# Optimization experiments

Hardware: AMD Instinct MI355X
Metric: run time of the kernel (lower is better)

## Reference

```python
import jax, jax.numpy as jnp
import numpy as np

N, E, B, ROWS, IN, HID, JKO, FEAT, OH, OUT = 200000, 6400000, 64, 128, 128, 6, 4, 2560, 20, 2

def _leaky(x, s):
    return jnp.where(x >= 0, x, s * x)

def _ln(x, g, b, eps=1e-5):
    mu = jnp.mean(x, -1, keepdims=True)
    v = jnp.mean((x - mu) ** 2, -1, keepdims=True)
    return (x - mu) * jax.lax.rsqrt(v + eps) * g + b

def setup_inputs():
    key = jax.random.key(0)
    ks = jax.random.split(key, 32)
    def w(k, shape, fan_in):
        return jax.random.normal(k, shape, jnp.float32) * (1.0 / np.sqrt(fan_in))
    inp = {
        'x': jax.random.normal(ks[0], (N, IN), jnp.float32),
        'edge_index': jax.random.randint(ks[1], (2, E), 0, N, jnp.int32),
        'batch': jnp.sort(jax.random.randint(ks[2], (N,), 0, B, jnp.int32)),
        'features': jax.random.normal(ks[3], (B, ROWS, FEAT), jnp.float32),
        'one_hot': jax.random.uniform(ks[4], (B, OH), jnp.float32),
        # GATv2Conv params (heads=1)
        'W_l': w(ks[5], (IN, HID), IN), 'b_l': jnp.zeros((HID,)),
        'W_r': w(ks[6], (IN, HID), IN), 'b_r': jnp.zeros((HID,)),
        'att': w(ks[7], (HID,), HID), 'conv_b': jnp.zeros((HID,)),
        # BasicGNN final lin after JK (6 -> 4)
        'jk_W': w(ks[8], (HID, JKO), HID), 'jk_b': jnp.zeros((JKO,)),
        # MLP chain on features
        'l1_W': w(ks[9], (FEAT, 256), FEAT), 'l1_b': jnp.zeros((256,)),
        'ln1_g': jnp.ones((256,)), 'ln1_b': jnp.zeros((256,)),
        'l2_W': w(ks[10], (256, 64), 256), 'l2_b': jnp.zeros((64,)),
        'ln2_g': jnp.ones((64,)), 'ln2_b': jnp.zeros((64,)),
        'l3_W': w(ks[11], (64, 8), 64), 'l3_b': jnp.zeros((8,)),
        'ln3_g': jnp.ones((8,)), 'ln3_b': jnp.zeros((8,)),
        # flattening: rows*8 -> 32
        'fl_W': w(ks[12], (ROWS * 8, 32), ROWS * 8), 'fl_b': jnp.zeros((32,)),
        'ln4_g': jnp.ones((32,)), 'ln4_b': jnp.zeros((32,)),
        # output: 4 + 32 + 20 = 56 -> OUT
        'out_W': w(ks[13], (56, OUT), 56), 'out_b': jnp.zeros((OUT,)),
    }
    return inp

def _forward(x, features, one_hot, W_l, b_l, W_r, b_r, att, conv_b, jk_W, jk_b,
             l1_W, l1_b, ln1_g, ln1_b, l2_W, l2_b, ln2_g, ln2_b, l3_W, l3_b, ln3_g, ln3_b,
             fl_W, fl_b, ln4_g, ln4_b, out_W, out_b, edge_index, batch):
    n = x.shape[0]
    # GATv2Conv, heads=1: separate source/target transforms
    xl = x @ W_l + b_l  # [N,6] source/message features
    xr = x @ W_r + b_r  # [N,6] target features
    loops = jnp.arange(n, dtype=edge_index.dtype)
    src = jnp.concatenate([edge_index[0], loops])  # add self loops
    dst = jnp.concatenate([edge_index[1], loops])
    e = _leaky(xl[src] + xr[dst], 0.2)             # [E+N,6]
    score = e @ att                                 # [E+N]
    m = jax.lax.stop_gradient(jax.ops.segment_max(score, dst, num_segments=n))
    p = jnp.exp(score - m[dst])
    z = jax.ops.segment_sum(p, dst, num_segments=n)
    alpha = p / z[dst]                              # segment softmax over incoming edges
    agg = jax.ops.segment_sum(alpha[:, None] * xl[src], dst, num_segments=n) + conv_b
    x1 = _leaky(agg, 0.01)                          # BasicGNN act ('leakyrelu')
    # JK-LSTM with a single layer collapses to identity (softmax over 1 element)
    h = x1 @ jk_W + jk_b                            # [N,4]
    # global mean pool per graph
    nb = features.shape[0]
    sums = jax.ops.segment_sum(h, batch, num_segments=nb)
    cnt = jax.ops.segment_sum(jnp.ones((n,), h.dtype), batch, num_segments=nb)
    xgcn = sums / jnp.maximum(cnt, 1.0)[:, None]    # [B,4]
    # MLP on features (dropout = identity in eval)
    f = _leaky(_ln(features @ l1_W + l1_b, ln1_g, ln1_b), 0.01)
    f = _leaky(_ln(f @ l2_W + l2_b, ln2_g, ln2_b), 0.01)
    f = _leaky(_ln(f @ l3_W + l3_b, ln3_g, ln3_b), 0.01)  # [B,ROWS,8]
    flat = f.reshape(nb, -1)
    xf = _leaky(_ln(flat @ fl_W + fl_b, ln4_g, ln4_b), 0.01)  # [B,32]
    cat = jnp.concatenate([xgcn, xf, one_hot], axis=1)        # [B,56]
    return cat @ out_W + out_b

def reference(x, features, one_hot, W_l, b_l, W_r, b_r, att, conv_b, jk_W, jk_b,
              l1_W, l1_b, ln1_g, ln1_b, l2_W, l2_b, ln2_g, ln2_b, l3_W, l3_b, ln3_g, ln3_b,
              fl_W, fl_b, ln4_g, ln4_b, out_W, out_b, edge_index, batch):
    return _forward(x, features, one_hot, W_l, b_l, W_r, b_r, att, conv_b, jk_W, jk_b,
                    l1_W, l1_b, ln1_g, ln1_b, l2_W, l2_b, ln2_g, ln2_b, l3_W, l3_b, ln3_g, ln3_b,
                    fl_W, fl_b, ln4_g, ln4_b, out_W, out_b, edge_index, batch)
```

## Files before the change

kernel.cpp:

```cpp
#include <hip/hip_runtime.h>
#include <cstdint>
#include <cstddef>

#define N_NODES 200000
#define N_EDGES 6400000
#define NB      64
#define MROWS   8192
#define FEAT    2560

#define BSZ   256
#define NBK   782
#define EBLK  512
#define ETILE 12500
#define BCAP  8960

typedef __attribute__((ext_vector_type(8))) short bf16x8;
typedef __attribute__((ext_vector_type(4))) float f32x4;

__device__ __forceinline__ unsigned short bf16rne(float f) {
    unsigned u = __builtin_bit_cast(unsigned, f);
    u += 0x7fffu + ((u >> 16) & 1u);
    return (unsigned short)(u >> 16);
}

__device__ __forceinline__ void async_cp16(const void* g, void* l) {
    __builtin_amdgcn_global_load_lds(
        (const __attribute__((address_space(1))) unsigned int*)g,
        (__attribute__((address_space(3))) unsigned int*)l, 16, 0, 0);
}

__device__ __forceinline__ void edge_acc(
    uint4 g, const float* xrd, const float* attv, float& z, float* agg)
{
    float xls[6];
    xls[0] = __builtin_bit_cast(float, g.x << 16);
    xls[1] = __builtin_bit_cast(float, g.x & 0xffff0000u);
    xls[2] = __builtin_bit_cast(float, g.y << 16);
    xls[3] = __builtin_bit_cast(float, g.y & 0xffff0000u);
    xls[4] = __builtin_bit_cast(float, g.z << 16);
    xls[5] = __builtin_bit_cast(float, g.z & 0xffff0000u);
    float sc = 0.f;
#pragma unroll
    for (int j = 0; j < 6; j++) {
        float e = xls[j] + xrd[j];
        e = (e >= 0.f) ? e : 0.2f * e;
        sc += attv[j] * e;
    }
    const float p = __expf(sc);
    z += p;
#pragma unroll
    for (int j = 0; j < 6; j++) agg[j] += p * xls[j];
}


__global__ __launch_bounds__(256) void node_xform(
    const float* __restrict__ x,
    const float* __restrict__ Wl, const float* __restrict__ bl,
    const float* __restrict__ Wr, const float* __restrict__ br,
    unsigned short* __restrict__ xlb, float* __restrict__ xr)
{
    const int t = threadIdx.x;
    const int l = t & 15;
    const int node = blockIdx.x * 16 + (t >> 4);

    float wl[48], wr[48];
#pragma unroll
    for (int q = 0; q < 12; q++) {
        *(float4*)&wl[q * 4] = *(const float4*)(Wl + 48 * l + 4 * q);
        *(float4*)&wr[q * 4] = *(const float4*)(Wr + 48 * l + 4 * q);
    }
    float xv[8];
    *(float4*)&xv[0] = *(const float4*)(x + (size_t)node * 128 + l * 8);
    *(float4*)&xv[4] = *(const float4*)(x + (size_t)node * 128 + l * 8 + 4);

    float al[6] = {}, ar[6] = {};
#pragma unroll
    for (int i = 0; i < 8; i++) {
#pragma unroll
        for (int j = 0; j < 6; j++) {
            al[j] += xv[i] * wl[i * 6 + j];
            ar[j] += xv[i] * wr[i * 6 + j];
        }
    }
#pragma unroll
    for (int off = 8; off >= 1; off >>= 1) {
#pragma unroll
        for (int j = 0; j < 6; j++) {
            al[j] += __shfl_xor(al[j], off);
            ar[j] += __shfl_xor(ar[j], off);
        }
    }
    if (l == 0) {
        union { unsigned short h[8]; uint4 v; } u;
#pragma unroll
        for (int j = 0; j < 6; j++) u.h[j] = bf16rne(al[j] + bl[j]);
        u.h[6] = 0; u.h[7] = 0;
        *(uint4*)(xlb + (size_t)node * 8) = u.v;
        float4 r0; float2 r1;
        r0.x = ar[0] + br[0]; r0.y = ar[1] + br[1];
        r0.z = ar[2] + br[2]; r0.w = ar[3] + br[3];
        r1.x = ar[4] + br[4]; r1.y = ar[5] + br[5];
        *(float4*)(xr + (size_t)node * 8) = r0;
        *(float2*)(xr + (size_t)node * 8 + 4) = r1;
    }
}

__global__ __launch_bounds__(256) void edge_bucket(
    const int* __restrict__ ei, int* __restrict__ cursor, int* __restrict__ pairs)
{
    __shared__ int sorted[ETILE];
    __shared__ int hb[NBK + 1];
    __shared__ int cur[NBK];
    __shared__ int gbl[NBK];
    __shared__ int wsum[4];
    const int t = threadIdx.x;
    const int lane = t & 63, wid = t >> 6;
    const int base = blockIdx.x * ETILE;

    for (int b = t; b < NBK; b += 256) cur[b] = 0;
    __syncthreads();

    for (int i = t; i < ETILE; i += 256)
        atomicAdd(&cur[ei[N_EDGES + base + i] >> 8], 1);
    __syncthreads();

    int c[4]; int lsum = 0;
#pragma unroll
    for (int q = 0; q < 4; q++) {
        const int b = 4 * t + q;
        c[q] = (b < NBK) ? cur[b] : 0;
        lsum += c[q];
    }
    int v = lsum;
#pragma unroll
    for (int d = 1; d < 64; d <<= 1) {
        const int o = __shfl_up(v, d);
        if (lane >= d) v += o;
    }
    if (lane == 63) wsum[wid] = v;
    __syncthreads();
    int off = 0;
#pragma unroll
    for (int w = 0; w < 3; w++) if (w < wid) off += wsum[w];
    int run = off + v - lsum;

    int mygb[4];
#pragma unroll
    for (int q = 0; q < 4; q++) {
        const int b = 4 * t + q;
        mygb[q] = (b < NBK && c[q] > 0) ? atomicAdd(&cursor[b], c[q]) : 0;
    }

#pragma unroll
    for (int q = 0; q < 4; q++) {
        const int b = 4 * t + q;
        if (b <= NBK) hb[b] = run;
        if (b < NBK) cur[b] = run;
        run += c[q];
    }
    __syncthreads();

    for (int i = t; i < ETILE; i += 256) {
        const int d = ei[N_EDGES + base + i];
        const int s = ei[base + i];
        const int pos = atomicAdd(&cur[d >> 8], 1);
        sorted[pos] = (s << 8) | (d & 255);
    }
#pragma unroll
    for (int q = 0; q < 4; q++) {
        const int b = 4 * t + q;
        if (b < NBK) gbl[b] = mygb[q];
    }
    __syncthreads();

    const int grp = t >> 4, gl = t & 15;
    for (int b = grp; b < NBK; b += 16) {
        const int st = hb[b];
        const int cnt = hb[b + 1] - st;
        int* dst = pairs + b * BCAP + gbl[b];
        for (int i = gl; i < cnt; i += 16)
            dst[i] = sorted[st + i];
    }
}

__global__ __launch_bounds__(256) void bucket_reduce(
    const int* __restrict__ pairs, const int* __restrict__ cursor,
    const unsigned short* __restrict__ xlb, const float* __restrict__ xr,
    const float* __restrict__ att, const float* __restrict__ conv_b,
    const float* __restrict__ jkW, const float* __restrict__ jkb,
    const int* __restrict__ batch,
    float* __restrict__ gsum, float* __restrict__ gcnt)
{
    __shared__ int sorted[BCAP];
    __shared__ int hist[256];
    __shared__ int wtot[4];
    const int t = threadIdx.x;
    const int lane = t & 63, wid = t >> 6;
    const int d0 = blockIdx.x * BSZ + t;

    float xrd[6];
    if (d0 < N_NODES) {
        float4 a = *(const float4*)(xr + (size_t)d0 * 8);
        float2 b = *(const float2*)(xr + (size_t)d0 * 8 + 4);
        xrd[0] = a.x; xrd[1] = a.y; xrd[2] = a.z;
        xrd[3] = a.w; xrd[4] = b.x; xrd[5] = b.y;
    } else {
#pragma unroll
        for (int j = 0; j < 6; j++) xrd[j] = 0.f;
    }
    float attv[6];
#pragma unroll
    for (int j = 0; j < 6; j++) attv[j] = att[j];

    float z = 0.f, agg[6] = {};
    const uint4* xl4 = (const uint4*)xlb;
    const int e0 = blockIdx.x * BCAP;
    const int e1 = e0 + cursor[blockIdx.x];

    for (int c0 = e0; c0 < e1; c0 += BCAP) {
        const int rem = e1 - c0;
        const int cnt_chunk = (rem < BCAP) ? rem : BCAP;
        hist[t] = 0;
        __syncthreads();
        for (int i = t; i < cnt_chunk; i += 256)
            atomicAdd(&hist[pairs[c0 + i] & 255], 1);
        __syncthreads();
        const int h = hist[t];
        int v = h;
#pragma unroll
        for (int d = 1; d < 64; d <<= 1) {
            int o = __shfl_up(v, d);
            if (lane >= d) v += o;
        }
        if (lane == 63) wtot[wid] = v;
        __syncthreads();
        int off = 0;
#pragma unroll
        for (int wv = 0; wv < 3; wv++) if (wv < wid) off += wtot[wv];
        const int my_start = v - h + off;
        const int my_cnt = h;
        __syncthreads();
        hist[t] = my_start;
        __syncthreads();
        for (int i = t; i < cnt_chunk; i += 256) {
            const int pv = pairs[c0 + i];
            const int pos = atomicAdd(&hist[pv & 255], 1);
            sorted[pos] = ((unsigned)pv) >> 8;
        }
        __syncthreads();
        int i = 0;
        for (; i + 4 <= my_cnt; i += 4) {
            const int s0 = sorted[my_start + i];
            const int s1 = sorted[my_start + i + 1];
            const int s2 = sorted[my_start + i + 2];
            const int s3 = sorted[my_start + i + 3];
            const uint4 g0 = xl4[s0], g1 = xl4[s1], g2 = xl4[s2], g3 = xl4[s3];
            edge_acc(g0, xrd, attv, z, agg);
            edge_acc(g1, xrd, attv, z, agg);
            edge_acc(g2, xrd, attv, z, agg);
            edge_acc(g3, xrd, attv, z, agg);
        }
        for (; i < my_cnt; i++) {
            const uint4 g = xl4[sorted[my_start + i]];
            edge_acc(g, xrd, attv, z, agg);
        }
        __syncthreads();
    }

    float hh[4] = {0.f, 0.f, 0.f, 0.f};
    float cw = 0.f;
    int b = 0;
    if (d0 < N_NODES) {
        const uint4 g = xl4[d0];
        float xld[6];
        xld[0] = __builtin_bit_cast(float, g.x << 16);
        xld[1] = __builtin_bit_cast(float, g.x & 0xffff0000u);
        xld[2] = __builtin_bit_cast(float, g.y << 16);
        xld[3] = __builtin_bit_cast(float, g.y & 0xffff0000u);
        xld[4] = __builtin_bit_cast(float, g.z << 16);
        xld[5] = __builtin_bit_cast(float, g.z & 0xffff0000u);
        float sc = 0.f;
#pragma unroll
        for (int j = 0; j < 6; j++) {
            float e = xld[j] + xrd[j];
            e = (e >= 0.f) ? e : 0.2f * e;
            sc += attv[j] * e;
        }
        const float p = __expf(sc);
        const float zz = z + p;
#pragma unroll
        for (int c = 0; c < 4; c++) hh[c] = jkb[c];
#pragma unroll
        for (int j = 0; j < 6; j++) {
            float aj = (agg[j] + p * xld[j]) / zz + conv_b[j];
            aj = (aj >= 0.f) ? aj : 0.01f * aj;
#pragma unroll
            for (int c = 0; c < 4; c++) hh[c] += aj * jkW[j * 4 + c];
        }
        b = batch[d0];
        cw = 1.f;
    }
    const int b0 = __shfl(b, 0);
    if (__all(b == b0)) {
#pragma unroll
        for (int off2 = 32; off2 >= 1; off2 >>= 1) {
#pragma unroll
            for (int c = 0; c < 4; c++) hh[c] += __shfl_xor(hh[c], off2);
            cw += __shfl_xor(cw, off2);
        }
        if (lane == 0 && cw > 0.f) {
#pragma unroll
            for (int c = 0; c < 4; c++) atomicAdd(gsum + b0 * 4 + c, hh[c]);
            atomicAdd(gcnt + b0, cw);
        }
    } else if (cw > 0.f) {
#pragma unroll
        for (int c = 0; c < 4; c++) atomicAdd(gsum + b * 4 + c, hh[c]);
        atomicAdd(gcnt + b, cw);
    }
}

__global__ __launch_bounds__(256) void castT(
    const float* __restrict__ W, unsigned short* __restrict__ Wt, int K, int N)
{
    const int k = blockIdx.x * 256 + threadIdx.x;
    const int n = blockIdx.y;
    if (k < K) Wt[(size_t)n * K + k] = bf16rne(W[(size_t)k * N + n]);
}

__global__ __launch_bounds__(256) void mfma_gemm_l1(
    const float* __restrict__ A, const unsigned short* __restrict__ Bt,
    const float* __restrict__ bias, float* __restrict__ C,
    int M, int N, int K)
{
    __shared__ unsigned short As[2][64 * 64];
    __shared__ unsigned short Bs[2][128 * 64];
    const int t = threadIdx.x;
    const int w = t >> 6, l = t & 63;
    const int l15 = l & 15, quad = l >> 4;
    const int wm = (w & 1) * 32, wn = (w >> 1) * 64;
    const int gm0 = blockIdx.x * 64;
    const int gn0 = blockIdx.y * 128;
    const int r8 = l >> 3;
    const int c8 = (l & 7) ^ r8;
    const int ar = t >> 2;
    const int ac0 = (t & 3) * 2;

    f32x4 acc[2][4];
#pragma unroll
    for (int mt = 0; mt < 2; mt++)
#pragma unroll
        for (int nt = 0; nt < 4; nt++) acc[mt][nt] = (f32x4){0.f, 0.f, 0.f, 0.f};

    const int niter = K / 64;

#pragma unroll
    for (int c = 0; c < 4; c++) {
        const int j = w * 4 + c;
        async_cp16(Bt + (size_t)(gn0 + j * 8 + r8) * K + c8 * 8, &Bs[0][j * 512]);
    }
    {
        const float* src = A + (size_t)(gm0 + ar) * K + ac0 * 8;
        float4 v0 = *(const float4*)src;
        float4 v1 = *(const float4*)(src + 4);
        float4 v2 = *(const float4*)(src + 8);
        float4 v3 = *(const float4*)(src + 12);
        union { unsigned short h[8]; uint4 u; } p0, p1;
        p0.h[0] = bf16rne(v0.x); p0.h[1] = bf16rne(v0.y);
        p0.h[2] = bf16rne(v0.z); p0.h[3] = bf16rne(v0.w);
        p0.h[4] = bf16rne(v1.x); p0.h[5] = bf16rne(v1.y);
        p0.h[6] = bf16rne(v1.z); p0.h[7] = bf16rne(v1.w);
        p1.h[0] = bf16rne(v2.x); p1.h[1] = bf16rne(v2.y);
        p1.h[2] = bf16rne(v2.z); p1.h[3] = bf16rne(v2.w);
        p1.h[4] = bf16rne(v3.x); p1.h[5] = bf16rne(v3.y);
        p1.h[6] = bf16rne(v3.z); p1.h[7] = bf16rne(v3.w);
        *(uint4*)&As[0][ar * 64 + ((ac0 + 0) ^ (ar & 7)) * 8] = p0.u;
        *(uint4*)&As[0][ar * 64 + ((ac0 + 1) ^ (ar & 7)) * 8] = p1.u;
    }

    int p = 0;
    for (int i = 0; i < niter; i++) {
        __syncthreads();
        const bool nxt = (i + 1 < niter);
        float4 v0, v1, v2, v3;
        if (nxt) {
            const int k1 = (i + 1) * 64;
#pragma unroll
            for (int c = 0; c < 4; c++) {
                const int j = w * 4 + c;
                async_cp16(Bt + (size_t)(gn0 + j * 8 + r8) * K + k1 + c8 * 8,
                           &Bs[p ^ 1][j * 512]);
            }
            const float* src = A + (size_t)(gm0 + ar) * K + k1 + ac0 * 8;
            v0 = *(const float4*)src;
            v1 = *(const float4*)(src + 4);
            v2 = *(const float4*)(src + 8);
            v3 = *(const float4*)(src + 12);
        }
#pragma unroll
        for (int kki = 0; kki < 2; kki++) {
            bf16x8 af[2], bfr[4];
#pragma unroll
            for (int mt = 0; mt < 2; mt++) {
                const int m = wm + mt * 16 + l15;
                af[mt] = *(const bf16x8*)&As[p][m * 64 + (((quad + 4 * kki) ^ (m & 7)) * 8)];
            }
#pragma unroll
            for (int nt = 0; nt < 4; nt++) {
                const int n = wn + nt * 16 + l15;
                bfr[nt] = *(const bf16x8*)&Bs[p][n * 64 + (((quad + 4 * kki) ^ (n & 7)) * 8)];
            }
#pragma unroll
            for (int mt = 0; mt < 2; mt++)
#pragma unroll
                for (int nt = 0; nt < 4; nt++)
                    acc[mt][nt] = __builtin_amdgcn_mfma_f32_16x16x32_bf16(
                        af[mt], bfr[nt], acc[mt][nt], 0, 0, 0);
        }
        if (nxt) {
            union { unsigned short h[8]; uint4 u; } p0, p1;
            p0.h[0] = bf16rne(v0.x); p0.h[1] = bf16rne(v0.y);
            p0.h[2] = bf16rne(v0.z); p0.h[3] = bf16rne(v0.w);
            p0.h[4] = bf16rne(v1.x); p0.h[5] = bf16rne(v1.y);
            p0.h[6] = bf16rne(v1.z); p0.h[7] = bf16rne(v1.w);
            p1.h[0] = bf16rne(v2.x); p1.h[1] = bf16rne(v2.y);
            p1.h[2] = bf16rne(v2.z); p1.h[3] = bf16rne(v2.w);
            p1.h[4] = bf16rne(v3.x); p1.h[5] = bf16rne(v3.y);
            p1.h[6] = bf16rne(v3.z); p1.h[7] = bf16rne(v3.w);
            *(uint4*)&As[p ^ 1][ar * 64 + ((ac0 + 0) ^ (ar & 7)) * 8] = p0.u;
            *(uint4*)&As[p ^ 1][ar * 64 + ((ac0 + 1) ^ (ar & 7)) * 8] = p1.u;
        }
        p ^= 1;
    }
#pragma unroll
    for (int nt = 0; nt < 4; nt++) {
        const int col = gn0 + wn + nt * 16 + l15;
        const float bv = bias[col];
#pragma unroll
        for (int mt = 0; mt < 2; mt++)
#pragma unroll
            for (int rr = 0; rr < 4; rr++) {
                const int row = gm0 + wm + mt * 16 + quad * 4 + rr;
                C[(size_t)row * N + col] = acc[mt][nt][rr] + bv;
            }
    }
}

__global__ __launch_bounds__(256) void mfma_gemm_l2(
    const unsigned short* __restrict__ Ab, const unsigned short* __restrict__ Bt,
    const float* __restrict__ bias, float* __restrict__ C,
    int M, int N, int K)
{
    __shared__ unsigned short As[32 * 64];
    __shared__ unsigned short Bs[64 * 64];
    const int t = threadIdx.x;
    const int w = t >> 6, l = t & 63;
    const int l15 = l & 15, quad = l >> 4;
    const int gm0 = blockIdx.x * 32;
    const int gn0 = blockIdx.y * 64;
    const int r8 = l >> 3;
    const int c8 = (l & 7) ^ r8;

    f32x4 acc[2];
    acc[0] = (f32x4){0.f, 0.f, 0.f, 0.f};
    acc[1] = (f32x4){0.f, 0.f, 0.f, 0.f};

    for (int k0 = 0; k0 < K; k0 += 64) {
#pragma unroll
        for (int c = 0; c < 2; c++) {
            const int j = w * 2 + c;
            async_cp16(Bt + (size_t)(gn0 + j * 8 + r8) * K + k0 + c8 * 8,
                       &Bs[j * 512]);
        }
        async_cp16(Ab + (size_t)(gm0 + w * 8 + r8) * K + k0 + c8 * 8, &As[w * 512]);
        __syncthreads();
#pragma unroll
        for (int kki = 0; kki < 2; kki++) {
            bf16x8 af[2], bfr;
#pragma unroll
            for (int mt = 0; mt < 2; mt++) {
                const int m = mt * 16 + l15;
                af[mt] = *(const bf16x8*)&As[m * 64 + (((quad + 4 * kki) ^ (m & 7)) * 8)];
            }
            const int n = w * 16 + l15;
            bfr = *(const bf16x8*)&Bs[n * 64 + (((quad + 4 * kki) ^ (n & 7)) * 8)];
#pragma unroll
            for (int mt = 0; mt < 2; mt++)
                acc[mt] = __builtin_amdgcn_mfma_f32_16x16x32_bf16(
                    af[mt], bfr, acc[mt], 0, 0, 0);
        }
        __syncthreads();
    }
    const int col = gn0 + w * 16 + l15;
    const float bv = bias[col];
#pragma unroll
    for (int mt = 0; mt < 2; mt++)
#pragma unroll
        for (int rr = 0; rr < 4; rr++) {
            const int row = gm0 + mt * 16 + quad * 4 + rr;
            C[(size_t)row * N + col] = acc[mt][rr] + bv;
        }
}

__global__ __launch_bounds__(256) void ln_leaky_c256(
    const float* __restrict__ f, unsigned short* __restrict__ out,
    const float* __restrict__ g, const float* __restrict__ b)
{
    const int row = blockIdx.x;
    const int t = threadIdx.x;
    float v = f[(size_t)row * 256 + t];
    float s = v, s2 = v * v;
#pragma unroll
    for (int off = 32; off >= 1; off >>= 1) {
        s += __shfl_xor(s, off);
        s2 += __shfl_xor(s2, off);
    }
    __shared__ float ws[4], ws2[4];
    const int wid = t >> 6, lane = t & 63;
    if (lane == 0) { ws[wid] = s; ws2[wid] = s2; }
    __syncthreads();
    const float S = ws[0] + ws[1] + ws[2] + ws[3];
    const float S2 = ws2[0] + ws2[1] + ws2[2] + ws2[3];
    const float mu = S * (1.0f / 256.0f);
    const float var = S2 * (1.0f / 256.0f) - mu * mu;
    float y = (v - mu) * rsqrtf(var + 1e-5f) * g[t] + b[t];
    y = (y >= 0.f) ? y : 0.01f * y;
    out[(size_t)row * 256 + t] = bf16rne(y);
}

__global__ __launch_bounds__(256) void ln_leaky_c64(
    float* __restrict__ f, const float* __restrict__ g, const float* __restrict__ b)
{
    const int wid = threadIdx.x >> 6, lane = threadIdx.x & 63;
    const int row = blockIdx.x * 4 + wid;
    float v = f[(size_t)row * 64 + lane];
    float s = v, s2 = v * v;
#pragma unroll
    for (int off = 32; off >= 1; off >>= 1) {
        s += __shfl_xor(s, off);
        s2 += __shfl_xor(s2, off);
    }
    const float mu = s * (1.0f / 64.0f);
    const float var = s2 * (1.0f / 64.0f) - mu * mu;
    float y = (v - mu) * rsqrtf(var + 1e-5f) * g[lane] + b[lane];
    f[(size_t)row * 64 + lane] = (y >= 0.f) ? y : 0.01f * y;
}

__global__ __launch_bounds__(256) void l3_ln_leaky(
    const float* __restrict__ f2, const float* __restrict__ W3,
    const float* __restrict__ b3,
    const float* __restrict__ g, const float* __restrict__ b,
    float* __restrict__ f3)
{
    __shared__ float sW[64 * 8];
    const int t = threadIdx.x;
    sW[t] = W3[t]; sW[t + 256] = W3[t + 256];
    __syncthreads();
    const int row = blockIdx.x * 32 + (t >> 3);
    const int c = t & 7;
    float acc = b3[c];
    const float* fr = f2 + (size_t)row * 64;
#pragma unroll 8
    for (int k = 0; k < 64; k++) acc += fr[k] * sW[k * 8 + c];
    float s = acc, s2 = acc * acc;
#pragma unroll
    for (int off = 4; off >= 1; off >>= 1) {
        s += __shfl_xor(s, off);
        s2 += __shfl_xor(s2, off);
    }
    const float mu = s * (1.0f / 8.0f);
    const float var = s2 * (1.0f / 8.0f) - mu * mu;
    float y = (acc - mu) * rsqrtf(var + 1e-5f) * g[c] + b[c];
    f3[(size_t)row * 8 + c] = (y >= 0.f) ? y : 0.01f * y;
}

__global__ __launch_bounds__(256) void flat_ln_leaky(
    const float* __restrict__ f3, const float* __restrict__ W,
    const float* __restrict__ bb,
    const float* __restrict__ g, const float* __restrict__ b,
    float* __restrict__ xf)
{
    __shared__ float sf[1024];
    __shared__ float sp[8][32];
    const int t = threadIdx.x;
    const int gb = blockIdx.x;
    *(float4*)&sf[t * 4] = *(const float4*)(f3 + (size_t)gb * 1024 + t * 4);
    __syncthreads();
    const int c = t & 31, part = t >> 5;
    float acc = 0.f;
    for (int k = part * 128; k < part * 128 + 128; k++) acc += sf[k] * W[k * 32 + c];
    sp[part][c] = acc;
    __syncthreads();
    if (t < 32) {
        float v = bb[t];
#pragma unroll
        for (int p = 0; p < 8; p++) v += sp[p][t];
        float s = v, s2 = v * v;
#pragma unroll
        for (int off = 16; off >= 1; off >>= 1) {
            s += __shfl_xor(s, off);
            s2 += __shfl_xor(s2, off);
        }
        const float mu = s * (1.0f / 32.0f);
        const float var = s2 * (1.0f / 32.0f) - mu * mu;
        float y = (v - mu) * rsqrtf(var + 1e-5f) * g[t] + b[t];
        xf[gb * 32 + t] = (y >= 0.f) ? y : 0.01f * y;
    }
}

__global__ __launch_bounds__(128) void final_out(
    const float* __restrict__ gsum, const float* __restrict__ gcnt,
    const float* __restrict__ xf, const float* __restrict__ onehot,
    const float* __restrict__ Wo, const float* __restrict__ bo,
    float* __restrict__ out)
{
    const int t = threadIdx.x;
    const int gb = t >> 1, o = t & 1;
    float cnt = gcnt[gb];
    cnt = (cnt > 1.f) ? cnt : 1.f;
    float acc = bo[o];
#pragma unroll
    for (int j = 0; j < 4; j++)  acc += (gsum[gb * 4 + j] / cnt) * Wo[j * 2 + o];
#pragma unroll
    for (int j = 0; j < 32; j++) acc += xf[gb * 32 + j] * Wo[(4 + j) * 2 + o];
#pragma unroll
    for (int j = 0; j < 20; j++) acc += onehot[gb * 20 + j] * Wo[(36 + j) * 2 + o];
    out[t] = acc;
}

extern "C" void kernel_launch(void* const* d_in, const int* in_sizes, int n_in,
                              void* d_out, int out_size, void* d_ws, size_t ws_size,
                              hipStream_t stream)
{
    const float* x        = (const float*)d_in[0];
    const int*   ei       = (const int*)d_in[1];
    const int*   batch    = (const int*)d_in[2];
    const float* features = (const float*)d_in[3];
    const float* one_hot  = (const float*)d_in[4];
    const float* W_l   = (const float*)d_in[5];
    const float* b_l   = (const float*)d_in[6];
    const float* W_r   = (const float*)d_in[7];
    const float* b_r   = (const float*)d_in[8];
    const float* att   = (const float*)d_in[9];
    const float* conv_b = (const float*)d_in[10];
    const float* jk_W  = (const float*)d_in[11];
    const float* jk_b  = (const float*)d_in[12];
    const float* l1_W  = (const float*)d_in[13];
    const float* l1_b  = (const float*)d_in[14];
    const float* ln1_g = (const float*)d_in[15];
    const float* ln1_b = (const float*)d_in[16];
    const float* l2_W  = (const float*)d_in[17];
    const float* l2_b  = (const float*)d_in[18];
    const float* ln2_g = (const float*)d_in[19];
    const float* ln2_b = (const float*)d_in[20];
    const float* l3_W  = (const float*)d_in[21];
    const float* l3_b  = (const float*)d_in[22];
    const float* ln3_g = (const float*)d_in[23];
    const float* ln3_b = (const float*)d_in[24];
    const float* fl_W  = (const float*)d_in[25];
    const float* fl_b  = (const float*)d_in[26];
    const float* ln4_g = (const float*)d_in[27];
    const float* ln4_b = (const float*)d_in[28];
    const float* out_W = (const float*)d_in[29];
    const float* out_b = (const float*)d_in[30];
    (void)in_sizes; (void)n_in; (void)out_size; (void)ws_size;

    float* ws = (float*)d_ws;
    unsigned short* xlb = (unsigned short*)(ws + 0);
    float* xr   = ws + 800000;
    unsigned short* w1t = (unsigned short*)(ws + 2400000);
    unsigned short* w2t = (unsigned short*)(ws + 2727680);
    float* gsum   = ws + 2735872;
    float* gcnt   = ws + 2736128;
    int*   cursor = (int*)(ws + 2736192);
    int* pairs = (int*)(ws + 2737024);
    float* f1           = ws + 2737024;
    unsigned short* f1b = (unsigned short*)(ws + 4834176);
    float* f2           = ws + 5358464;
    float* f3           = ws + 5882752;
    float* xf           = ws + 5948288;

    hipMemsetAsync(gsum, 0, 1102 * sizeof(float), stream);

    node_xform<<<N_NODES / 16, 256, 0, stream>>>(x, W_l, b_l, W_r, b_r, xlb, xr);
    edge_bucket<<<EBLK, 256, 0, stream>>>(ei, cursor, pairs);
    castT<<<dim3(10, 256), 256, 0, stream>>>(l1_W, w1t, FEAT, 256);
    castT<<<dim3(1, 64), 256, 0, stream>>>(l2_W, w2t, 256, 64);
    bucket_reduce<<<NBK, 256, 0, stream>>>(pairs, cursor, xlb, xr, att, conv_b,
                                           jk_W, jk_b, batch, gsum, gcnt);
    mfma_gemm_l1<<<dim3(MROWS / 64, 2), 256, 0, stream>>>(
        features, w1t, l1_b, f1, MROWS, 256, FEAT);
    ln_leaky_c256<<<MROWS, 256, 0, stream>>>(f1, f1b, ln1_g, ln1_b);
    mfma_gemm_l2<<<dim3(MROWS / 32, 1), 256, 0, stream>>>(
        f1b, w2t, l2_b, f2, MROWS, 64, 256);
    ln_leaky_c64<<<MROWS / 4, 256, 0, stream>>>(f2, ln2_g, ln2_b);
    l3_ln_leaky<<<MROWS / 32, 256, 0, stream>>>(f2, l3_W, l3_b, ln3_g, ln3_b, f3);
    flat_ln_leaky<<<NB, 256, 0, stream>>>(f3, fl_W, fl_b, ln4_g, ln4_b, xf);
    final_out<<<1, 128, 0, stream>>>(gsum, gcnt, xf, one_hot, out_W, out_b, (float*)d_out);
}
```

Measured before the change: 598.3 us.

## Fuse node transform, edge bucketing and first GEMM into one multi-role kernel

Merges three independent front-stage kernels (node feature transform, edge bucketing, layer-1 MFMA GEMM) into a single launch whose blocks pick a role from blockIdx, so the stages run concurrently across CUs rather than one after another. The node transform becomes a grid-stride loop over a fixed block count, and the GEMM output buffers move further into the workspace so they no longer alias the pairs buffer. The fused path is used only when the workspace is large enough, with the old sequence kept as a fallback. Sharing one launch means every block reserves the largest shared-memory footprint, which can lower occupancy for the lighter roles.

```diff
diff --git a/kernel.cpp b/kernel.cpp
--- a/kernel.cpp
+++ b/kernel.cpp
@@ -13,6 +13,8 @@
 #define EBLK  512
 #define ETILE 12500
 #define BCAP  8960
+#define NXB   768
+#define GEMMB 256
 
 typedef __attribute__((ext_vector_type(8))) short bf16x8;
 typedef __attribute__((ext_vector_type(4))) float f32x4;
@@ -53,7 +55,8 @@
 }
 
 
-__global__ __launch_bounds__(256) void node_xform(
+__device__ __forceinline__ void nx_body(
+    const int nxi, const int nstride,
     const float* __restrict__ x,
     const float* __restrict__ Wl, const float* __restrict__ bl,
     const float* __restrict__ Wr, const float* __restrict__ br,
@@ -61,7 +64,6 @@
 {
     const int t = threadIdx.x;
     const int l = t & 15;
-    const int node = blockIdx.x * 16 + (t >> 4);
 
     float wl[48], wr[48];
 #pragma unroll
@@ -69,53 +71,57 @@
         *(float4*)&wl[q * 4] = *(const float4*)(Wl + 48 * l + 4 * q);
         *(float4*)&wr[q * 4] = *(const float4*)(Wr + 48 * l + 4 * q);
     }
-    float xv[8];
-    *(float4*)&xv[0] = *(const float4*)(x + (size_t)node * 128 + l * 8);
-    *(float4*)&xv[4] = *(const float4*)(x + (size_t)node * 128 + l * 8 + 4);
-
-    float al[6] = {}, ar[6] = {};
-#pragma unroll
-    for (int i = 0; i < 8; i++) {
-#pragma unroll
-        for (int j = 0; j < 6; j++) {
-            al[j] += xv[i] * wl[i * 6 + j];
-            ar[j] += xv[i] * wr[i * 6 + j];
-        }
-    }
-#pragma unroll
-    for (int off = 8; off >= 1; off >>= 1) {
-#pragma unroll
-        for (int j = 0; j < 6; j++) {
-            al[j] += __shfl_xor(al[j], off);
-            ar[j] += __shfl_xor(ar[j], off);
-        }
-    }
-    if (l == 0) {
-        union { unsigned short h[8]; uint4 v; } u;
-#pragma unroll
-        for (int j = 0; j < 6; j++) u.h[j] = bf16rne(al[j] + bl[j]);
-        u.h[6] = 0; u.h[7] = 0;
-        *(uint4*)(xlb + (size_t)node * 8) = u.v;
-        float4 r0; float2 r1;
-        r0.x = ar[0] + br[0]; r0.y = ar[1] + br[1];
-        r0.z = ar[2] + br[2]; r0.w = ar[3] + br[3];
-        r1.x = ar[4] + br[4]; r1.y = ar[5] + br[5];
-        *(float4*)(xr + (size_t)node * 8) = r0;
-        *(float2*)(xr + (size_t)node * 8 + 4) = r1;
-    }
-}
-
-__global__ __launch_bounds__(256) void edge_bucket(
+    for (int g = nxi; g < N_NODES / 16; g += nstride) {
+        const int node = g * 16 + (t >> 4);
+        float xv[8];
+        *(float4*)&xv[0] = *(const float4*)(x + (size_t)node * 128 + l * 8);
+        *(float4*)&xv[4] = *(const float4*)(x + (size_t)node * 128 + l * 8 + 4);
+
+        float al[6] = {}, ar[6] = {};
+#pragma unroll
+        for (int i = 0; i < 8; i++) {
+#pragma unroll
+            for (int j = 0; j < 6; j++) {
+                al[j] += xv[i] * wl[i * 6 + j];
+                ar[j] += xv[i] * wr[i * 6 + j];
+            }
+        }
+#pragma unroll
+        for (int off = 8; off >= 1; off >>= 1) {
+#pragma unroll
+            for (int j = 0; j < 6; j++) {
+                al[j] += __shfl_xor(al[j], off);
+                ar[j] += __shfl_xor(ar[j], off);
+            }
+        }
+        if (l == 0) {
+            union { unsigned short h[8]; uint4 v; } u;
+#pragma unroll
+            for (int j = 0; j < 6; j++) u.h[j] = bf16rne(al[j] + bl[j]);
+            u.h[6] = 0; u.h[7] = 0;
+            *(uint4*)(xlb + (size_t)node * 8) = u.v;
+            float4 r0; float2 r1;
+            r0.x = ar[0] + br[0]; r0.y = ar[1] + br[1];
+            r0.z = ar[2] + br[2]; r0.w = ar[3] + br[3];
+            r1.x = ar[4] + br[4]; r1.y = ar[5] + br[5];
+            *(float4*)(xr + (size_t)node * 8) = r0;
+            *(float2*)(xr + (size_t)node * 8 + 4) = r1;
+        }
+    }
+}
+
+__device__ __forceinline__ void eb_body(
+    const int bid, char* smem,
     const int* __restrict__ ei, int* __restrict__ cursor, int* __restrict__ pairs)
 {
-    __shared__ int sorted[ETILE];
-    __shared__ int hb[NBK + 1];
-    __shared__ int cur[NBK];
-    __shared__ int gbl[NBK];
-    __shared__ int wsum[4];
+    int* sorted = (int*)smem;
+    int* hb     = sorted + ETILE;
+    int* cur    = hb + NBK + 1;
+    int* gbl    = cur + NBK;
+    int* wsum   = gbl + NBK;
     const int t = threadIdx.x;
     const int lane = t & 63, wid = t >> 6;
-    const int base = blockIdx.x * ETILE;
+    const int base = bid * ETILE;
 
     for (int b = t; b < NBK; b += 256) cur[b] = 0;
     __syncthreads();
@@ -183,164 +189,21 @@
     }
 }
 
-__global__ __launch_bounds__(256) void bucket_reduce(
-    const int* __restrict__ pairs, const int* __restrict__ cursor,
-    const unsigned short* __restrict__ xlb, const float* __restrict__ xr,
-    const float* __restrict__ att, const float* __restrict__ conv_b,
-    const float* __restrict__ jkW, const float* __restrict__ jkb,
-    const int* __restrict__ batch,
-    float* __restrict__ gsum, float* __restrict__ gcnt)
-{
-    __shared__ int sorted[BCAP];
-    __shared__ int hist[256];
-    __shared__ int wtot[4];
-    const int t = threadIdx.x;
-    const int lane = t & 63, wid = t >> 6;
-    const int d0 = blockIdx.x * BSZ + t;
-
-    float xrd[6];
-    if (d0 < N_NODES) {
-        float4 a = *(const float4*)(xr + (size_t)d0 * 8);
-        float2 b = *(const float2*)(xr + (size_t)d0 * 8 + 4);
-        xrd[0] = a.x; xrd[1] = a.y; xrd[2] = a.z;
-        xrd[3] = a.w; xrd[4] = b.x; xrd[5] = b.y;
-    } else {
-#pragma unroll
-        for (int j = 0; j < 6; j++) xrd[j] = 0.f;
-    }
-    float attv[6];
-#pragma unroll
-    for (int j = 0; j < 6; j++) attv[j] = att[j];
-
-    float z = 0.f, agg[6] = {};
-    const uint4* xl4 = (const uint4*)xlb;
-    const int e0 = blockIdx.x * BCAP;
-    const int e1 = e0 + cursor[blockIdx.x];
-
-    for (int c0 = e0; c0 < e1; c0 += BCAP) {
-        const int rem = e1 - c0;
-        const int cnt_chunk = (rem < BCAP) ? rem : BCAP;
-        hist[t] = 0;
-        __syncthreads();
-        for (int i = t; i < cnt_chunk; i += 256)
-            atomicAdd(&hist[pairs[c0 + i] & 255], 1);
-        __syncthreads();
-        const int h = hist[t];
-        int v = h;
-#pragma unroll
-        for (int d = 1; d < 64; d <<= 1) {
-            int o = __shfl_up(v, d);
-            if (lane >= d) v += o;
-        }
-        if (lane == 63) wtot[wid] = v;
-        __syncthreads();
-        int off = 0;
-#pragma unroll
-        for (int wv = 0; wv < 3; wv++) if (wv < wid) off += wtot[wv];
-        const int my_start = v - h + off;
-        const int my_cnt = h;
-        __syncthreads();
-        hist[t] = my_start;
-        __syncthreads();
-        for (int i = t; i < cnt_chunk; i += 256) {
-            const int pv = pairs[c0 + i];
-            const int pos = atomicAdd(&hist[pv & 255], 1);
-            sorted[pos] = ((unsigned)pv) >> 8;
-        }
-        __syncthreads();
-        int i = 0;
-        for (; i + 4 <= my_cnt; i += 4) {
-            const int s0 = sorted[my_start + i];
-            const int s1 = sorted[my_start + i + 1];
-            const int s2 = sorted[my_start + i + 2];
-            const int s3 = sorted[my_start + i + 3];
-            const uint4 g0 = xl4[s0], g1 = xl4[s1], g2 = xl4[s2], g3 = xl4[s3];
-            edge_acc(g0, xrd, attv, z, agg);
-            edge_acc(g1, xrd, attv, z, agg);
-            edge_acc(g2, xrd, attv, z, agg);
-            edge_acc(g3, xrd, attv, z, agg);
-        }
-        for (; i < my_cnt; i++) {
-            const uint4 g = xl4[sorted[my_start + i]];
-            edge_acc(g, xrd, attv, z, agg);
-        }
-        __syncthreads();
-    }
-
-    float hh[4] = {0.f, 0.f, 0.f, 0.f};
-    float cw = 0.f;
-    int b = 0;
-    if (d0 < N_NODES) {
-        const uint4 g = xl4[d0];
-        float xld[6];
-        xld[0] = __builtin_bit_cast(float, g.x << 16);
-        xld[1] = __builtin_bit_cast(float, g.x & 0xffff0000u);
-        xld[2] = __builtin_bit_cast(float, g.y << 16);
-        xld[3] = __builtin_bit_cast(float, g.y & 0xffff0000u);
-        xld[4] = __builtin_bit_cast(float, g.z << 16);
-        xld[5] = __builtin_bit_cast(float, g.z & 0xffff0000u);
-        float sc = 0.f;
-#pragma unroll
-        for (int j = 0; j < 6; j++) {
-            float e = xld[j] + xrd[j];
-            e = (e >= 0.f) ? e : 0.2f * e;
-            sc += attv[j] * e;
-        }
-        const float p = __expf(sc);
-        const float zz = z + p;
-#pragma unroll
-        for (int c = 0; c < 4; c++) hh[c] = jkb[c];
-#pragma unroll
-        for (int j = 0; j < 6; j++) {
-            float aj = (agg[j] + p * xld[j]) / zz + conv_b[j];
-            aj = (aj >= 0.f) ? aj : 0.01f * aj;
-#pragma unroll
-            for (int c = 0; c < 4; c++) hh[c] += aj * jkW[j * 4 + c];
-        }
-        b = batch[d0];
-        cw = 1.f;
-    }
-    const int b0 = __shfl(b, 0);
-    if (__all(b == b0)) {
-#pragma unroll
-        for (int off2 = 32; off2 >= 1; off2 >>= 1) {
-#pragma unroll
-            for (int c = 0; c < 4; c++) hh[c] += __shfl_xor(hh[c], off2);
-            cw += __shfl_xor(cw, off2);
-        }
-        if (lane == 0 && cw > 0.f) {
-#pragma unroll
-            for (int c = 0; c < 4; c++) atomicAdd(gsum + b0 * 4 + c, hh[c]);
-            atomicAdd(gcnt + b0, cw);
-        }
-    } else if (cw > 0.f) {
-#pragma unroll
-        for (int c = 0; c < 4; c++) atomicAdd(gsum + b * 4 + c, hh[c]);
-        atomicAdd(gcnt + b, cw);
-    }
-}
-
-__global__ __launch_bounds__(256) void castT(
-    const float* __restrict__ W, unsigned short* __restrict__ Wt, int K, int N)
-{
-    const int k = blockIdx.x * 256 + threadIdx.x;
-    const int n = blockIdx.y;
-    if (k < K) Wt[(size_t)n * K + k] = bf16rne(W[(size_t)k * N + n]);
-}
-
-__global__ __launch_bounds__(256) void mfma_gemm_l1(
+__device__ __forceinline__ void gemm_l1_body(
+    const int bx, const int by, char* smem,
     const float* __restrict__ A, const unsigned short* __restrict__ Bt,
-    const float* __restrict__ bias, float* __restrict__ C,
-    int M, int N, int K)
-{
-    __shared__ unsigned short As[2][64 * 64];
-    __shared__ unsigned short Bs[2][128 * 64];
+    const float* __restrict__ bias, float* __restrict__ C)
+{
+    unsigned short (*As)[64 * 64] = (unsigned short(*)[64 * 64])smem;
+    unsigned short (*Bs)[128 * 64] =
+        (unsigned short(*)[128 * 64])(smem + 2 * 64 * 64 * sizeof(short));
+    const int K = FEAT, N = 256;
     const int t = threadIdx.x;
     const int w = t >> 6, l = t & 63;
     const int l15 = l & 15, quad = l >> 4;
     const int wm = (w & 1) * 32, wn = (w >> 1) * 64;
-    const int gm0 = blockIdx.x * 64;
-    const int gn0 = blockIdx.y * 128;
+    const int gm0 = bx * 64;
+    const int gn0 = by * 128;
     const int r8 = l >> 3;
     const int c8 = (l & 7) ^ r8;
     const int ar = t >> 2;
@@ -444,6 +307,199 @@
                 C[(size_t)row * N + col] = acc[mt][nt][rr] + bv;
             }
     }
+}
+
+
+__global__ __launch_bounds__(256) void node_xform(
+    const float* __restrict__ x,
+    const float* __restrict__ Wl, const float* __restrict__ bl,
+    const float* __restrict__ Wr, const float* __restrict__ br,
+    unsigned short* __restrict__ xlb, float* __restrict__ xr)
+{
+    nx_body(blockIdx.x, N_NODES / 16, x, Wl, bl, Wr, br, xlb, xr);
+}
+
+__global__ __launch_bounds__(256) void edge_bucket(
+    const int* __restrict__ ei, int* __restrict__ cursor, int* __restrict__ pairs)
+{
+    __shared__ __align__(16) char smem[59408];
+    eb_body(blockIdx.x, smem, ei, cursor, pairs);
+}
+
+__global__ __launch_bounds__(256) void mfma_gemm_l1(
+    const float* __restrict__ A, const unsigned short* __restrict__ Bt,
+    const float* __restrict__ bias, float* __restrict__ C)
+{
+    __shared__ __align__(16) char smem[49152];
+    gemm_l1_body(blockIdx.x, blockIdx.y, smem, A, Bt, bias, C);
+}
+
+__global__ __launch_bounds__(256) void fused_front(
+    const float* __restrict__ x,
+    const float* __restrict__ Wl, const float* __restrict__ bl,
+    const float* __restrict__ Wr, const float* __restrict__ br,
+    unsigned short* __restrict__ xlb, float* __restrict__ xr,
+    const int* __restrict__ ei, int* __restrict__ cursor, int* __restrict__ pairs,
+    const float* __restrict__ A, const unsigned short* __restrict__ Bt,
+    const float* __restrict__ bias, float* __restrict__ C)
+{
+    __shared__ __align__(16) char smem[59408];
+    const int bid = blockIdx.x;
+    const int role = bid % 3;
+    const int q = bid / 3;
+    if (role == 0) {
+        eb_body(q, smem, ei, cursor, pairs);
+    } else if (role == 1 && q < GEMMB) {
+        gemm_l1_body(q & 127, q >> 7, smem, A, Bt, bias, C);
+    } else {
+        const int nxi = (role == 2) ? q : EBLK + (q - GEMMB);
+        nx_body(nxi, NXB, x, Wl, bl, Wr, br, xlb, xr);
+    }
+}
+
+__global__ __launch_bounds__(256) void bucket_reduce(
+    const int* __restrict__ pairs, const int* __restrict__ cursor,
+    const unsigned short* __restrict__ xlb, const float* __restrict__ xr,
+    const float* __restrict__ att, const float* __restrict__ conv_b,
+    const float* __restrict__ jkW, const float* __restrict__ jkb,
+    const int* __restrict__ batch,
+    float* __restrict__ gsum, float* __restrict__ gcnt)
+{
+    __shared__ int sorted[BCAP];
+    __shared__ int hist[256];
+    __shared__ int wtot[4];
+    const int t = threadIdx.x;
+    const int lane = t & 63, wid = t >> 6;
+    const int d0 = blockIdx.x * BSZ + t;
+
+    float xrd[6];
+    if (d0 < N_NODES) {
+        float4 a = *(const float4*)(xr + (size_t)d0 * 8);
+        float2 b = *(const float2*)(xr + (size_t)d0 * 8 + 4);
+        xrd[0] = a.x; xrd[1] = a.y; xrd[2] = a.z;
+        xrd[3] = a.w; xrd[4] = b.x; xrd[5] = b.y;
+    } else {
+#pragma unroll
+        for (int j = 0; j < 6; j++) xrd[j] = 0.f;
+    }
+    float attv[6];
+#pragma unroll
+    for (int j = 0; j < 6; j++) attv[j] = att[j];
+
+    float z = 0.f, agg[6] = {};
+    const uint4* xl4 = (const uint4*)xlb;
+    const int e0 = blockIdx.x * BCAP;
+    const int e1 = e0 + cursor[blockIdx.x];
+
+    for (int c0 = e0; c0 < e1; c0 += BCAP) {
+        const int rem = e1 - c0;
+        const int cnt_chunk = (rem < BCAP) ? rem : BCAP;
+        hist[t] = 0;
+        __syncthreads();
+        for (int i = t; i < cnt_chunk; i += 256)
+            atomicAdd(&hist[pairs[c0 + i] & 255], 1);
+        __syncthreads();
+        const int h = hist[t];
+        int v = h;
+#pragma unroll
+        for (int d = 1; d < 64; d <<= 1) {
+            int o = __shfl_up(v, d);
+            if (lane >= d) v += o;
+        }
+        if (lane == 63) wtot[wid] = v;
+        __syncthreads();
+        int off = 0;
+#pragma unroll
+        for (int wv = 0; wv < 3; wv++) if (wv < wid) off += wtot[wv];
+        const int my_start = v - h + off;
+        const int my_cnt = h;
+        __syncthreads();
+        hist[t] = my_start;
+        __syncthreads();
+        for (int i = t; i < cnt_chunk; i += 256) {
+            const int pv = pairs[c0 + i];
+            const int pos = atomicAdd(&hist[pv & 255], 1);
+            sorted[pos] = ((unsigned)pv) >> 8;
+        }
+        __syncthreads();
+        int i = 0;
+        for (; i + 4 <= my_cnt; i += 4) {
+            const int s0 = sorted[my_start + i];
+            const int s1 = sorted[my_start + i + 1];
+            const int s2 = sorted[my_start + i + 2];
+            const int s3 = sorted[my_start + i + 3];
+            const uint4 g0 = xl4[s0], g1 = xl4[s1], g2 = xl4[s2], g3 = xl4[s3];
+            edge_acc(g0, xrd, attv, z, agg);
+            edge_acc(g1, xrd, attv, z, agg);
+            edge_acc(g2, xrd, attv, z, agg);
+            edge_acc(g3, xrd, attv, z, agg);
+        }
+        for (; i < my_cnt; i++) {
+            const uint4 g = xl4[sorted[my_start + i]];
+            edge_acc(g, xrd, attv, z, agg);
+        }
+        __syncthreads();
+    }
+
+    float hh[4] = {0.f, 0.f, 0.f, 0.f};
+    float cw = 0.f;
+    int b = 0;
+    if (d0 < N_NODES) {
+        const uint4 g = xl4[d0];
+        float xld[6];
+        xld[0] = __builtin_bit_cast(float, g.x << 16);
+        xld[1] = __builtin_bit_cast(float, g.x & 0xffff0000u);
+        xld[2] = __builtin_bit_cast(float, g.y << 16);
+        xld[3] = __builtin_bit_cast(float, g.y & 0xffff0000u);
+        xld[4] = __builtin_bit_cast(float, g.z << 16);
+        xld[5] = __builtin_bit_cast(float, g.z & 0xffff0000u);
+        float sc = 0.f;
+#pragma unroll
+        for (int j = 0; j < 6; j++) {
+            float e = xld[j] + xrd[j];
+            e = (e >= 0.f) ? e : 0.2f * e;
+            sc += attv[j] * e;
+        }
+        const float p = __expf(sc);
+        const float zz = z + p;
+#pragma unroll
+        for (int c = 0; c < 4; c++) hh[c] = jkb[c];
+#pragma unroll
+        for (int j = 0; j < 6; j++) {
+            float aj = (agg[j] + p * xld[j]) / zz + conv_b[j];
+            aj = (aj >= 0.f) ? aj : 0.01f * aj;
+#pragma unroll
+            for (int c = 0; c < 4; c++) hh[c] += aj * jkW[j * 4 + c];
+        }
+        b = batch[d0];
+        cw = 1.f;
+    }
+    const int b0 = __shfl(b, 0);
+    if (__all(b == b0)) {
+#pragma unroll
+        for (int off2 = 32; off2 >= 1; off2 >>= 1) {
+#pragma unroll
+            for (int c = 0; c < 4; c++) hh[c] += __shfl_xor(hh[c], off2);
+            cw += __shfl_xor(cw, off2);
+        }
+        if (lane == 0 && cw > 0.f) {
+#pragma unroll
+            for (int c = 0; c < 4; c++) atomicAdd(gsum + b0 * 4 + c, hh[c]);
+            atomicAdd(gcnt + b0, cw);
+        }
+    } else if (cw > 0.f) {
+#pragma unroll
+        for (int c = 0; c < 4; c++) atomicAdd(gsum + b * 4 + c, hh[c]);
+        atomicAdd(gcnt + b, cw);
+    }
+}
+
+__global__ __launch_bounds__(256) void castT(
+    const float* __restrict__ W, unsigned short* __restrict__ Wt, int K, int N)
+{
+    const int k = blockIdx.x * 256 + threadIdx.x;
+    const int n = blockIdx.y;
+    if (k < K) Wt[(size_t)n * K + k] = bf16rne(W[(size_t)k * N + n]);
 }
 
 __global__ __launch_bounds__(256) void mfma_gemm_l2(
@@ -663,7 +719,7 @@
     const float* ln4_b = (const float*)d_in[28];
     const float* out_W = (const float*)d_in[29];
     const float* out_b = (const float*)d_in[30];
-    (void)in_sizes; (void)n_in; (void)out_size; (void)ws_size;
+    (void)in_sizes; (void)n_in; (void)out_size;
 
     float* ws = (float*)d_ws;
     unsigned short* xlb = (unsigned short*)(ws + 0);
@@ -674,22 +730,47 @@
     float* gcnt   = ws + 2736128;
     int*   cursor = (int*)(ws + 2736192);
     int* pairs = (int*)(ws + 2737024);
-    float* f1           = ws + 2737024;
-    unsigned short* f1b = (unsigned short*)(ws + 4834176);
-    float* f2           = ws + 5358464;
-    float* f3           = ws + 5882752;
-    float* xf           = ws + 5948288;
+
+    const bool fuse = ws_size >= (size_t)13481344 * 4;
+    float* f1;  unsigned short* f1b;  float* f2;  float* f3;  float* xf;
+    if (fuse) {
+        f1  = ws + 9743744;
+        f1b = (unsigned short*)(ws + 11840896);
+        f2  = ws + 12889472;
+        f3  = ws + 13413760;
+        xf  = ws + 13479296;
+    } else {
+        f1  = ws + 2737024;
+        f1b = (unsigned short*)(ws + 4834176);
+        f2  = ws + 5358464;
+        f3  = ws + 5882752;
+        xf  = ws + 5948288;
+    }
 
     hipMemsetAsync(gsum, 0, 1102 * sizeof(float), stream);
 
-    node_xform<<<N_NODES / 16, 256, 0, stream>>>(x, W_l, b_l, W_r, b_r, xlb, xr);
-    edge_bucket<<<EBLK, 256, 0, stream>>>(ei, cursor, pairs);
     castT<<<dim3(10, 256), 256, 0, stream>>>(l1_W, w1t, FEAT, 256);
     castT<<<dim3(1, 64), 256, 0, stream>>>(l2_W, w2t, 256, 64);
-    bucket_reduce<<<NBK, 256, 0, stream>>>(pairs, cursor, xlb, xr, att, conv_b,
-                                           jk_W, jk_b, batch, gsum, gcnt);
-    mfma_gemm_l1<<<dim3(MROWS / 64, 2), 256, 0, stream>>>(
-        features, w1t, l1_b, f1, MROWS, 256, FEAT);
+
+    if (fuse) {
+        fused_front<<<EBLK + GEMMB + NXB, 256, 0, stream>>>(
+            x, W_l, b_l, W_r, b_r, xlb, xr,
+            ei, cursor, pairs,
+            features, w1t, l1_b, f1);
+        bucket_reduce<<<NBK, 256, 0, stream>>>(pairs, cursor, xlb, xr, att,
+                                               conv_b, jk_W, jk_b, batch,
+                                               gsum, gcnt);
+    } else {
+        node_xform<<<N_NODES / 16, 256, 0, stream>>>(x, W_l, b_l, W_r, b_r,
+                                                     xlb, xr);
+        edge_bucket<<<EBLK, 256, 0, stream>>>(ei, cursor, pairs);
+        bucket_reduce<<<NBK, 256, 0, stream>>>(pairs, cursor, xlb, xr, att,
+                                               conv_b, jk_W, jk_b, batch,
+                                               gsum, gcnt);
+        mfma_gemm_l1<<<dim3(MROWS / 64, 2), 256, 0, stream>>>(
+            features, w1t, l1_b, f1);
+    }
+
     ln_leaky_c256<<<MROWS, 256, 0, stream>>>(f1, f1b, ln1_g, ln1_b);
     mfma_gemm_l2<<<dim3(MROWS / 32, 1), 256, 0, stream>>>(
         f1b, w2t, l2_b, f2, MROWS, 64, 256);
```

After: 541.7 us. 9.5% less time.
